# Performance work log

Measured on AMD Instinct MI355X. Metric: run time of the kernel, lower is better.

Reference implementation:

```python
import jax, jax.numpy as jnp
import numpy as np

B = 2          # point-cloud batches
N_PER_B = 8192 # non-empty pillars per batch
C = 128        # channels
H = 4          # heads
K = 4096       # max_tokens (top-k cap)
LN_EPS = 1e-5


def setup_inputs() -> dict:
    key = jax.random.key(0)
    ks = jax.random.split(key, 6)
    N = B * N_PER_B
    feats = jax.random.normal(ks[0], (N, C), dtype=jnp.float32)
    # equal-sized contiguous batch groups (sorted batch ids)
    batch_idx = jnp.repeat(jnp.arange(B, dtype=jnp.int64), N_PER_B)
    in_proj_w = jax.random.normal(ks[1], (3 * C, C), dtype=jnp.float32) * 0.02
    in_proj_b = jax.random.normal(ks[2], (3 * C,), dtype=jnp.float32) * 0.02
    out_proj_w = jax.random.normal(ks[3], (C, C), dtype=jnp.float32) * 0.02
    out_proj_b = jax.random.normal(ks[4], (C,), dtype=jnp.float32) * 0.02
    ln_w = jnp.ones((C,), dtype=jnp.float32)
    ln_b = jnp.zeros((C,), dtype=jnp.float32)
    return {"feats": feats, "batch_idx": batch_idx, "in_proj_w": in_proj_w,
            "in_proj_b": in_proj_b, "out_proj_w": out_proj_w,
            "out_proj_b": out_proj_b, "ln_w": ln_w, "ln_b": ln_b}


def _sparse_pillar_attn(feats, in_proj_w, in_proj_b, out_proj_w, out_proj_b, ln_w, ln_b):
    Dh = C // H
    x = feats.reshape(B, N_PER_B, C)
    # top-K tokens per batch by L2 feature norm (cap at max_tokens)
    norms = jnp.linalg.norm(x, axis=-1)                      # [B, n]
    _, topk = jax.lax.top_k(norms, K)                        # [B, K]
    xa = jnp.take_along_axis(x, topk[..., None], axis=1)     # [B, K, C]
    # MultiheadAttention (batch_first, self-attn)
    qkv = xa @ in_proj_w.T + in_proj_b                       # [B, K, 3C]
    q, k, v = jnp.split(qkv, 3, axis=-1)
    def heads(t):  # [B, K, C] -> [B, H, K, Dh]
        return t.reshape(B, K, H, Dh).transpose(0, 2, 1, 3)
    q, k, v = heads(q), heads(k), heads(v)
    scores = jnp.einsum('bhqd,bhkd->bhqk', q, k) / jnp.sqrt(jnp.float32(Dh))
    attn = jax.nn.softmax(scores, axis=-1)
    o = jnp.einsum('bhqk,bhkd->bhqd', attn, v)               # [B, H, K, Dh]
    o = o.transpose(0, 2, 1, 3).reshape(B, K, C)
    o = o @ out_proj_w.T + out_proj_b
    # residual + LayerNorm (dropout p=0 -> identity)
    h = xa + o
    mu = jnp.mean(h, axis=-1, keepdims=True)
    var = jnp.mean(jnp.square(h - mu), axis=-1, keepdims=True)
    y = (h - mu) / jnp.sqrt(var + LN_EPS) * ln_w + ln_b      # [B, K, C]
    # scatter back; non-selected tokens unchanged
    gidx = (jnp.arange(B)[:, None] * N_PER_B + topk).reshape(-1)
    return feats.at[gidx].set(y.reshape(-1, C))


def reference(feats, batch_idx, in_proj_w, in_proj_b, out_proj_w, out_proj_b, ln_w, ln_b):
    # batch_idx is sorted with equal group sizes, so groups are contiguous
    return _sparse_pillar_attn(feats, in_proj_w, in_proj_b, out_proj_w, out_proj_b, ln_w, ln_b)
```

## Files before the change

### kernel.cpp

```cpp
#include <hip/hip_runtime.h>
#include <hip/hip_bf16.h>
#include <stdint.h>

#define NPB 8192
#define CB 2
#define CC 128
#define HH 4
#define KTOK 4096
#define DH 32
#define NTOK (CB*KTOK)
#define K2C 0.25503402f

typedef __attribute__((ext_vector_type(8))) short sh8;
typedef __attribute__((ext_vector_type(4))) float fx4;
typedef __attribute__((ext_vector_type(16))) float fx16;
typedef __attribute__((ext_vector_type(2))) uint32_t ux2;
typedef __attribute__((ext_vector_type(4))) uint32_t ux4;

__device__ inline uint16_t f2bf(float f){
  uint32_t x = __float_as_uint(f);
  return (uint16_t)((x + 0x7FFFu + ((x>>16)&1u)) >> 16);
}
__device__ inline uint32_t pk2(float a, float b){
  return (uint32_t)f2bf(a) | ((uint32_t)f2bf(b) << 16);
}
__device__ inline float fast_exp2(float x){
#if __has_builtin(__builtin_amdgcn_exp2f)
  return __builtin_amdgcn_exp2f(x);
#else
  return exp2f(x);
#endif
}
__device__ inline uint32_t cvtpk1(float a, float b){
  uint32_t u;
  asm("v_cvt_pk_bf16_f32 %0, %1, %2" : "=v"(u) : "v"(a), "v"(b));
  return u;
}
__device__ inline fx4 mfma32(sh8 a, sh8 b, fx4 c){
  return __builtin_amdgcn_mfma_f32_16x16x32_bf16(a, b, c, 0, 0, 0);
}
__device__ inline fx16 mfma32x32(sh8 a, sh8 b, fx16 c){
  return __builtin_amdgcn_mfma_f32_32x32x16_bf16(a, b, c, 0, 0, 0);
}
__device__ inline void gload_lds(const uint16_t* g, uint16_t* l){
  __builtin_amdgcn_global_load_lds(
      (const __attribute__((address_space(1))) uint32_t*)g,
      (__attribute__((address_space(3))) uint32_t*)l,
      16, 0, 0);
}

__global__ __launch_bounds__(256) void k_cpnw(const float* __restrict__ feats,
                                              float* __restrict__ out,
                                              uint32_t* __restrict__ keys,
                                              const float* __restrict__ wq,
                                              const float* __restrict__ wo,
                                              uint16_t* __restrict__ wqb,
                                              uint16_t* __restrict__ wob){
  int bx = blockIdx.x;
  if (bx < 1024){
    int wv = threadIdx.x >> 6, lane = threadIdx.x & 63;
    int row0 = bx*16 + wv*4;
#pragma unroll
    for (int r = 0; r < 4; ++r){
      int row = row0 + r;
      float2 v = *(const float2*)(feats + row*CC + lane*2);
      *(float2*)(out + row*CC + lane*2) = v;
      float s = v.x*v.x + v.y*v.y;
      for (int m = 1; m < 64; m <<= 1) s += __shfl_xor(s, m);
      if (lane == 0) keys[row] = __float_as_uint(s);
    }
  } else {
    int i = (bx - 1024)*256 + threadIdx.x;
    if (i < 3*CC*CC) wqb[i] = f2bf(wq[i]);
    else { int j = i - 3*CC*CC; wob[j] = f2bf(wo[j]); }
  }
}

__global__ __launch_bounds__(1024) void k_select(const uint32_t* __restrict__ keys,
                                                 int* __restrict__ sel){
  __shared__ uint32_t ka[NPB];
  __shared__ uint32_t hist[16*257];
  __shared__ uint32_t sh_prefix, sh_r;
  __shared__ int wsum[17];
  int tid = threadIdx.x, batch = blockIdx.x;
  int wv16 = tid >> 6;
  for (int i = tid; i < NPB; i += 1024) ka[i] = keys[batch*NPB + i];
  if (tid == 0){ sh_prefix = 0u; sh_r = KTOK; }
  __syncthreads();
  for (int pass = 0; pass < 4; ++pass){
    int shift = 24 - 8*pass;
    for (int i = tid; i < 16*257; i += 1024) hist[i] = 0u;
    __syncthreads();
    uint32_t pref = sh_prefix;
    uint32_t r0   = sh_r;
    uint32_t mask = (pass == 0) ? 0u : (0xFFFFFFFFu << (shift + 8));
    uint32_t* myh = &hist[wv16*257];
    for (int e = 0; e < 8; ++e){
      uint32_t k = ka[tid*8 + e];
      if ((k & mask) == pref) atomicAdd(&myh[(k >> shift) & 255], 1u);
    }
    __syncthreads();
    if (tid < 64){
      int lane = tid;
      uint32_t h0v = 0, h1v = 0, h2v = 0, h3v = 0;
      int b0 = lane*4;
#pragma unroll
      for (int w = 0; w < 16; ++w){
        const uint32_t* hw = &hist[w*257 + b0];
        h0v += hw[0]; h1v += hw[1]; h2v += hw[2]; h3v += hw[3];
      }
      uint32_t s3 = h3v, s2 = h2v + s3, s1 = h1v + s2, s0 = h0v + s1;
      uint32_t incl = s0;
      for (int d = 1; d < 64; d <<= 1){
        uint32_t t = __shfl_down(incl, d);
        if (lane + d < 64) incl += t;
      }
      uint32_t exA = incl - s0;
      uint32_t sfx[4] = {s0, s1, s2, s3};
      uint32_t hh[4]  = {h0v, h1v, h2v, h3v};
#pragma unroll
      for (int k = 0; k < 4; ++k){
        uint32_t inc_b = exA + sfx[k];
        uint32_t Sx    = inc_b - hh[k];
        if (Sx < r0 && inc_b >= r0){
          sh_prefix = pref | ((uint32_t)(b0 + k) << shift);
          sh_r = r0 - Sx;
        }
      }
    }
    __syncthreads();
  }
  uint32_t T = sh_prefix; int need = (int)sh_r;
  int lgt = 0, leq = 0;
  for (int e = 0; e < 8; ++e){
    uint32_t k = ka[tid*8 + e];
    lgt += (k > T); leq += (k == T);
  }
  int lane = tid & 63, wv = tid >> 6;
  int egt, tgt, eeq;
  {
    __syncthreads();
    int incl = lgt;
    for (int d = 1; d < 64; d <<= 1){ int t = __shfl_up(incl, d); if (lane >= d) incl += t; }
    if (lane == 63) wsum[wv] = incl;
    __syncthreads();
    if (tid == 0){ int run = 0; for (int w = 0; w < 16; ++w){ int t = wsum[w]; wsum[w] = run; run += t; } wsum[16] = run; }
    __syncthreads();
    egt = wsum[wv] + incl - lgt; tgt = wsum[16];
  }
  {
    __syncthreads();
    int incl = leq;
    for (int d = 1; d < 64; d <<= 1){ int t = __shfl_up(incl, d); if (lane >= d) incl += t; }
    if (lane == 63) wsum[wv] = incl;
    __syncthreads();
    if (tid == 0){ int run = 0; for (int w = 0; w < 16; ++w){ int t = wsum[w]; wsum[w] = run; run += t; } }
    __syncthreads();
    eeq = wsum[wv] + incl - leq;
  }
  int chi = tgt, gpos = egt, epos = eeq;
  for (int e = 0; e < 8; ++e){
    int i = tid*8 + e;
    uint32_t k = ka[i];
    if (k > T){ sel[batch*KTOK + (gpos++)] = batch*NPB + i; }
    else if (k == T){ if (epos < need) sel[batch*KTOK + chi + epos] = batch*NPB + i; epos++; }
  }
}

__global__ __launch_bounds__(256) void k_qkv(const float* __restrict__ feats,
                                             const int* __restrict__ sel,
                                             const uint16_t* __restrict__ wqb,
                                             const float* __restrict__ bias,
                                             uint16_t* __restrict__ Qg,
                                             uint16_t* __restrict__ Kg,
                                             uint16_t* __restrict__ Vt){
  int wave = threadIdx.x >> 6, lane = threadIdx.x & 63;
  int l15 = lane & 15, g = lane >> 4;
  int rt = blockIdx.x;
  int arow = rt*16 + l15;
  int grow = sel[arow];
  sh8 aF[4];
#pragma unroll
  for (int kk = 0; kk < 4; ++kk){
    const float* src = feats + grow*CC + kk*32 + g*8;
    float4 v0 = *(const float4*)(src);
    float4 v1 = *(const float4*)(src + 4);
    ux4 u;
    u.x = cvtpk1(v0.x, v0.y);
    u.y = cvtpk1(v0.z, v0.w);
    u.z = cvtpk1(v1.x, v1.y);
    u.w = cvtpk1(v1.z, v1.w);
    aF[kk] = *(sh8*)&u;
  }
  int tbase = rt*16;
  int b  = tbase >> 12;
  int q0 = (tbase & 4095) + g*4;
#pragma unroll
  for (int cg = 0; cg < 6; ++cg){
    int bcol = (cg*4 + wave)*16 + l15;
    fx4 acc = {0.f,0.f,0.f,0.f};
#pragma unroll
    for (int kk = 0; kk < 4; ++kk){
      sh8 bF = *(const sh8*)(wqb + bcol*CC + kk*32 + g*8);
      acc = mfma32(aF[kk], bF, acc);
    }
    int j = bcol;
    float bj = bias[j];
    if (j < CC){
      int h = j >> 5, d = j & 31;
      uint16_t* p = Qg + ((b*HH + h)*KTOK + q0)*DH + d;
#pragma unroll
      for (int i = 0; i < 4; ++i) p[i*DH] = f2bf((acc[i] + bj) * K2C);
    } else if (j < 2*CC){
      int jj = j - CC; int h = jj >> 5, d = jj & 31;
      uint16_t* p = Kg + ((b*HH + h)*KTOK + q0)*DH + d;
#pragma unroll
      for (int i = 0; i < 4; ++i) p[i*DH] = f2bf(acc[i] + bj);
    } else {
      int jj = j - 2*CC; int h = jj >> 5, d = jj & 31;
      uint16_t* p = Vt + ((b*HH + h)*DH + d)*KTOK + q0;
      ux2 w; w.x = pk2(acc[0]+bj, acc[1]+bj); w.y = pk2(acc[2]+bj, acc[3]+bj);
      *(ux2*)p = w;
    }
  }
}

__global__ __launch_bounds__(1024) void k_attn(const uint16_t* __restrict__ Qg,
                                               const uint16_t* __restrict__ Kg,
                                               const uint16_t* __restrict__ Vtg,
                                               uint16_t* __restrict__ O){
  __shared__ __align__(16) char lds[68096];
  int tid = threadIdx.x;
  int wv = tid >> 6, lane = tid & 63;
  int l31 = lane & 31, hi = lane >> 5;
  int seg = wv & 3, tq = wv >> 2;
  int bh = blockIdx.y;
  int qt = blockIdx.x;
  const uint16_t* Qp = Qg  + bh*KTOK*DH;
  const uint16_t* Kp = Kg  + bh*KTOK*DH;
  const uint16_t* Vp = Vtg + bh*DH*KTOK;
  int q = qt*128 + tq*32 + l31;
  sh8 qF0 = *(const sh8*)(Qp + q*DH + hi*8);
  sh8 qF1 = *(const sh8*)(Qp + q*DH + 16 + hi*8);

  uint16_t* st = (uint16_t*)lds;
  int r16 = lane >> 2;
  int kr  = (r16 & 3) | ((r16 & 4) << 1) | ((r16 & 8) >> 1);
  int sx  = ((lane & 3) ^ ((r16 >> 1) & 3)) * 8;
  int sseg = wv & 3;
  int skey0 = sseg*1024;

  if (wv < 4){
    const uint16_t* kg = Kp + skey0*DH;
    uint16_t* d = st + sseg*4096;
#pragma unroll
    for (int ks = 0; ks < 2; ++ks){
      gload_lds(kg + (ks*32 + kr)*DH + sx,      d + ks*1024 + 0);
      gload_lds(kg + (ks*32 + 16 + kr)*DH + sx, d + ks*1024 + 512);
    }
  } else if (wv < 8){
    const uint16_t* vg = Vp + skey0;
    uint16_t* d = st + sseg*4096 + 2048;
#pragma unroll
    for (int ks = 0; ks < 2; ++ks){
      gload_lds(vg + r16*KTOK + ks*32 + sx,        d + ks*1024 + 0);
      gload_lds(vg + (16+r16)*KTOK + ks*32 + sx,   d + ks*1024 + 512);
    }
  }
  asm volatile("s_waitcnt vmcnt(0)" ::: "memory");
  __syncthreads();

  fx16 acc  = {0,0,0,0,0,0,0,0,0,0,0,0,0,0,0,0};
  fx16 accl = {0,0,0,0,0,0,0,0,0,0,0,0,0,0,0,0};
  const fx16 z16 = {0,0,0,0,0,0,0,0,0,0,0,0,0,0,0,0};
  const short ONEB = (short)0x3F80;
  sh8 onesB = {ONEB,ONEB,ONEB,ONEB,ONEB,ONEB,ONEB,ONEB};
  int swz = (l31 >> 1) & 3;
  int koff0 = l31*32 + ((hi     ^ swz)*8);
  int koff1 = l31*32 + (((hi+2) ^ swz)*8);

  for (int t = 0; t < 16; ++t){
    int b = t & 1;
    if (t < 15){
      int nk = skey0 + (t+1)*64;
      if (wv < 4){
        const uint16_t* kg = Kp + nk*DH;
        uint16_t* d = st + ((b^1)*4 + sseg)*4096;
#pragma unroll
        for (int ks = 0; ks < 2; ++ks){
          gload_lds(kg + (ks*32 + kr)*DH + sx,      d + ks*1024 + 0);
          gload_lds(kg + (ks*32 + 16 + kr)*DH + sx, d + ks*1024 + 512);
        }
      } else if (wv < 8){
        const uint16_t* vg = Vp + nk;
        uint16_t* d = st + ((b^1)*4 + sseg)*4096 + 2048;
#pragma unroll
        for (int ks = 0; ks < 2; ++ks){
          gload_lds(vg + r16*KTOK + ks*32 + sx,        d + ks*1024 + 0);
          gload_lds(vg + (16+r16)*KTOK + ks*32 + sx,   d + ks*1024 + 512);
        }
      }
    }
    const uint16_t* base = st + (b*4 + seg)*4096;
#pragma unroll
    for (int ks = 0; ks < 2; ++ks){
      const uint16_t* bK = base + ks*1024;
      const uint16_t* bV = base + 2048 + ks*1024;
      sh8 kA0 = *(const sh8*)(bK + koff0);
      sh8 kA1 = *(const sh8*)(bK + koff1);
      fx16 S = mfma32x32(kA0, qF0, z16);
      S = mfma32x32(kA1, qF1, S);
      float e[16];
#pragma unroll
      for (int r = 0; r < 16; ++r) e[r] = fast_exp2(S[r]);
      ux4 w0, w1;
      w0.x = cvtpk1(e[0],  e[1]);  w0.y = cvtpk1(e[2],  e[3]);
      w0.z = cvtpk1(e[4],  e[5]);  w0.w = cvtpk1(e[6],  e[7]);
      w1.x = cvtpk1(e[8],  e[9]);  w1.y = cvtpk1(e[10], e[11]);
      w1.z = cvtpk1(e[12], e[13]); w1.w = cvtpk1(e[14], e[15]);
      sh8 pa0 = *(sh8*)&w0;
      sh8 pa1 = *(sh8*)&w1;
      sh8 vB0 = *(const sh8*)(bV + koff0);
      sh8 vB1 = *(const sh8*)(bV + koff1);
      acc  = mfma32x32(pa0, vB0, acc);
      acc  = mfma32x32(pa1, vB1, acc);
      accl = mfma32x32(pa0, onesB, accl);
      accl = mfma32x32(pa1, onesB, accl);
    }
    asm volatile("s_waitcnt vmcnt(0)" ::: "memory");
    __syncthreads();
  }

  float* cmb = (float*)lds;
  float* lwp = (float*)(lds + 65536);
  float* ltr = (float*)(lds + 65536 + 2048);
#pragma unroll
  for (int i = 0; i < 16; i += 4){
    fx4 p = {acc[i], acc[i+1], acc[i+2], acc[i+3]};
    *(fx4*)&cmb[((tq*4 + seg)*64 + lane)*16 + i] = p;
  }
  if (l31 == 0){
#pragma unroll
    for (int r = 0; r < 16; ++r)
      lwp[wv*32 + (r&3) + 8*(r>>2) + 4*hi] = accl[r];
  }
  __syncthreads();
  if (seg == 0){
#pragma unroll
    for (int s = 1; s < 4; ++s){
#pragma unroll
      for (int i = 0; i < 16; i += 4){
        fx4 p = *(const fx4*)&cmb[((tq*4 + s)*64 + lane)*16 + i];
        acc[i] += p.x; acc[i+1] += p.y; acc[i+2] += p.z; acc[i+3] += p.w;
      }
    }
    float lt = (lwp[(tq*4+0)*32 + l31] + lwp[(tq*4+1)*32 + l31])
             + (lwp[(tq*4+2)*32 + l31] + lwp[(tq*4+3)*32 + l31]);
    if (!hi) ltr[tq*32 + l31] = lt;
    fx4 La = *(const fx4*)&ltr[tq*32 + 4*hi];
    fx4 Lb = *(const fx4*)&ltr[tq*32 + 8 + 4*hi];
    fx4 Lc = *(const fx4*)&ltr[tq*32 + 16 + 4*hi];
    fx4 Ld = *(const fx4*)&ltr[tq*32 + 24 + 4*hi];
    fx4 Ra = {1.f/La.x, 1.f/La.y, 1.f/La.z, 1.f/La.w};
    fx4 Rb = {1.f/Lb.x, 1.f/Lb.y, 1.f/Lb.z, 1.f/Lb.w};
    fx4 Rc = {1.f/Lc.x, 1.f/Lc.y, 1.f/Lc.z, 1.f/Lc.w};
    fx4 Rd = {1.f/Ld.x, 1.f/Ld.y, 1.f/Ld.z, 1.f/Ld.w};
    int bb = bh >> 2, h = bh & 3;
    uint16_t* op = O + (bb*KTOK + qt*128 + tq*32)*CC + h*DH + l31;
#pragma unroll
    for (int r = 0; r < 16; ++r){
      int qd = (r&3) + 8*(r>>2) + 4*hi;
      float rv = (r<4) ? Ra[r&3] : (r<8) ? Rb[r&3] : (r<12) ? Rc[r&3] : Rd[r&3];
      op[qd*CC] = f2bf(acc[r] * rv);
    }
  }
}

__global__ __launch_bounds__(256) void k_outln(const uint16_t* __restrict__ O,
                                               const uint16_t* __restrict__ wob,
                                               const float* __restrict__ bo,
                                               const float* __restrict__ feats,
                                               const int* __restrict__ sel,
                                               const float* __restrict__ lnw,
                                               const float* __restrict__ lnb,
                                               float* __restrict__ out){
  __shared__ float red[16][4][2];
  int wave = threadIdx.x >> 6, lane = threadIdx.x & 63;
  int l15 = lane & 15, g = lane >> 4;
  int rt = blockIdx.x;
  int arow = rt*16 + l15;
  int jA = wave*32 + l15, jB = jA + 16;
  fx4 accA = {0,0,0,0}, accB = {0,0,0,0};
#pragma unroll
  for (int kk = 0; kk < 4; ++kk){
    sh8 aF = *(const sh8*)(O   + arow*CC + kk*32 + g*8);
    sh8 b0 = *(const sh8*)(wob + jA*CC   + kk*32 + g*8);
    sh8 b1 = *(const sh8*)(wob + jB*CC   + kk*32 + g*8);
    accA = mfma32(aF, b0, accA);
    accB = mfma32(aF, b1, accB);
  }
  float bjA = bo[jA], bjB = bo[jB];
  float hA[4], hB[4]; int gl[4];
#pragma unroll
  for (int i = 0; i < 4; ++i){
    int r = rt*16 + g*4 + i;
    int grow = sel[r];
    gl[i] = grow;
    hA[i] = accA[i] + bjA + feats[grow*CC + jA];
    hB[i] = accB[i] + bjB + feats[grow*CC + jB];
  }
#pragma unroll
  for (int i = 0; i < 4; ++i){
    float s  = hA[i] + hB[i];
    float s2 = hA[i]*hA[i] + hB[i]*hB[i];
    for (int mk = 1; mk < 16; mk <<= 1){ s += __shfl_xor(s, mk); s2 += __shfl_xor(s2, mk); }
    if (l15 == 0){ red[g*4+i][wave][0] = s; red[g*4+i][wave][1] = s2; }
  }
  __syncthreads();
  float w0 = lnw[jA], w1 = lnw[jB], b0v = lnb[jA], b1v = lnb[jB];
#pragma unroll
  for (int i = 0; i < 4; ++i){
    int rl = g*4 + i;
    float tot  = red[rl][0][0] + red[rl][1][0] + red[rl][2][0] + red[rl][3][0];
    float tot2 = red[rl][0][1] + red[rl][1][1] + red[rl][2][1] + red[rl][3][1];
    float mu  = tot  * (1.f/128.f);
    float var = tot2 * (1.f/128.f) - mu*mu;
    float rs = rsqrtf(var + 1e-5f);
    out[gl[i]*CC + jA] = (hA[i]-mu)*rs*w0 + b0v;
    out[gl[i]*CC + jB] = (hB[i]-mu)*rs*w1 + b1v;
  }
}

extern "C" void kernel_launch(void* const* d_in, const int* in_sizes, int n_in,
                              void* d_out, int out_size, void* d_ws, size_t ws_size,
                              hipStream_t stream){
  const float* feats = (const float*)d_in[0];
  const float* wqkv  = (const float*)d_in[2];
  const float* bqkv  = (const float*)d_in[3];
  const float* wout  = (const float*)d_in[4];
  const float* bout  = (const float*)d_in[5];
  const float* lnw   = (const float*)d_in[6];
  const float* lnb   = (const float*)d_in[7];
  float* out = (float*)d_out;
  char* ws = (char*)d_ws;

  uint32_t* keys = (uint32_t*)(ws + 0);
  int*      sel  = (int*)     (ws + 65536);
  uint16_t* wqb  = (uint16_t*)(ws + 98304);
  uint16_t* wob  = (uint16_t*)(ws + 196608);
  uint16_t* Qg   = (uint16_t*)(ws + 2326528);
  uint16_t* Kg   = (uint16_t*)(ws + 4423680);
  uint16_t* Vt   = (uint16_t*)(ws + 6520832);
  uint16_t* O    = (uint16_t*)(ws + 8617984);

  hipLaunchKernelGGL(k_cpnw,   dim3(1280),   dim3(256),  0, stream,
                     feats, out, keys, wqkv, wout, wqb, wob);
  hipLaunchKernelGGL(k_select, dim3(2),      dim3(1024), 0, stream, keys, sel);
  hipLaunchKernelGGL(k_qkv,    dim3(512),    dim3(256),  0, stream,
                     feats, sel, wqb, bqkv, Qg, Kg, Vt);
  hipLaunchKernelGGL(k_attn,   dim3(32,8),   dim3(1024), 0, stream, Qg, Kg, Vt, O);
  hipLaunchKernelGGL(k_outln,  dim3(512),    dim3(256),  0, stream, O, wob, bout, feats, sel, lnw, lnb, out);
}
```

Baseline: 71.02 us.

## Copy only unselected rows in output kernel and move weight cast into select

The first kernel no longer copies all of feats into the output. It now only computes the row-norm keys and clears a selection-flag array. The select kernel marks the chosen rows in the flags and uses extra blocks to cast the weights to bf16. The output/LayerNorm kernel gets extra blocks that copy only the unselected rows, which avoids writing the selected half twice and takes the copy off the critical path at the start. The cost is that the flags array must be written and read, and the copy blocks now share the final kernel.

```diff
diff --git a/kernel.cpp b/kernel.cpp
--- a/kernel.cpp
+++ b/kernel.cpp
@@ -49,40 +49,36 @@
       16, 0, 0);
 }
 
-__global__ __launch_bounds__(256) void k_cpnw(const float* __restrict__ feats,
-                                              float* __restrict__ out,
-                                              uint32_t* __restrict__ keys,
-                                              const float* __restrict__ wq,
-                                              const float* __restrict__ wo,
-                                              uint16_t* __restrict__ wqb,
-                                              uint16_t* __restrict__ wob){
-  int bx = blockIdx.x;
-  if (bx < 1024){
-    int wv = threadIdx.x >> 6, lane = threadIdx.x & 63;
-    int row0 = bx*16 + wv*4;
-#pragma unroll
-    for (int r = 0; r < 4; ++r){
-      int row = row0 + r;
-      float2 v = *(const float2*)(feats + row*CC + lane*2);
-      *(float2*)(out + row*CC + lane*2) = v;
-      float s = v.x*v.x + v.y*v.y;
-      for (int m = 1; m < 64; m <<= 1) s += __shfl_xor(s, m);
-      if (lane == 0) keys[row] = __float_as_uint(s);
-    }
-  } else {
-    int i = (bx - 1024)*256 + threadIdx.x;
+__global__ __launch_bounds__(256) void k_norms(const float* __restrict__ feats,
+                                               uint32_t* __restrict__ keys,
+                                               int* __restrict__ flags){
+  if (blockIdx.x < 64) flags[blockIdx.x*256 + threadIdx.x] = 0;
+  int row  = blockIdx.x*4 + (threadIdx.x>>6);
+  int lane = threadIdx.x & 63;
+  float2 v = *(const float2*)(feats + row*CC + lane*2);
+  float s = v.x*v.x + v.y*v.y;
+  for (int m = 1; m < 64; m <<= 1) s += __shfl_xor(s, m);
+  if (lane == 0) keys[row] = __float_as_uint(s);
+}
+
+__global__ __launch_bounds__(1024) void k_select(const uint32_t* __restrict__ keys,
+                                                 int* __restrict__ sel,
+                                                 int* __restrict__ flags,
+                                                 const float* __restrict__ wq,
+                                                 const float* __restrict__ wo,
+                                                 uint16_t* __restrict__ wqb,
+                                                 uint16_t* __restrict__ wob){
+  int tid = threadIdx.x, batch = blockIdx.x;
+  if (batch >= 2){
+    int i = (batch - 2)*1024 + tid;
     if (i < 3*CC*CC) wqb[i] = f2bf(wq[i]);
     else { int j = i - 3*CC*CC; wob[j] = f2bf(wo[j]); }
-  }
-}
-
-__global__ __launch_bounds__(1024) void k_select(const uint32_t* __restrict__ keys,
-                                                 int* __restrict__ sel){
+    return;
+  }
   __shared__ uint32_t ka[NPB];
   __shared__ uint32_t hist[16*257];
   __shared__ uint32_t sh_prefix, sh_r;
   __shared__ int wsum[17];
-  int tid = threadIdx.x, batch = blockIdx.x;
   int wv16 = tid >> 6;
   for (int i = tid; i < NPB; i += 1024) ka[i] = keys[batch*NPB + i];
   if (tid == 0){ sh_prefix = 0u; sh_r = KTOK; }
@@ -162,8 +158,12 @@
   for (int e = 0; e < 8; ++e){
     int i = tid*8 + e;
     uint32_t k = ka[i];
-    if (k > T){ sel[batch*KTOK + (gpos++)] = batch*NPB + i; }
-    else if (k == T){ if (epos < need) sel[batch*KTOK + chi + epos] = batch*NPB + i; epos++; }
+    int grow = batch*NPB + i;
+    if (k > T){ sel[batch*KTOK + (gpos++)] = grow; flags[grow] = 1; }
+    else if (k == T){
+      if (epos < need){ sel[batch*KTOK + chi + epos] = grow; flags[grow] = 1; }
+      epos++;
+    }
   }
 }
 
@@ -381,13 +381,26 @@
                                                const float* __restrict__ bo,
                                                const float* __restrict__ feats,
                                                const int* __restrict__ sel,
+                                               const int* __restrict__ flags,
                                                const float* __restrict__ lnw,
                                                const float* __restrict__ lnb,
                                                float* __restrict__ out){
+  int bx = blockIdx.x;
+  if (bx >= 512){
+    int cb = bx - 512;
+    int row = cb*32 + (threadIdx.x >> 3);
+    int c0  = (threadIdx.x & 7) * 16;
+    if (!flags[row]){
+      const float4* s = (const float4*)(feats + row*CC + c0);
+      float4* d = (float4*)(out + row*CC + c0);
+      d[0] = s[0]; d[1] = s[1]; d[2] = s[2]; d[3] = s[3];
+    }
+    return;
+  }
   __shared__ float red[16][4][2];
   int wave = threadIdx.x >> 6, lane = threadIdx.x & 63;
   int l15 = lane & 15, g = lane >> 4;
-  int rt = blockIdx.x;
+  int rt = bx;
   int arow = rt*16 + l15;
   int jA = wave*32 + l15, jB = jA + 16;
   fx4 accA = {0,0,0,0}, accB = {0,0,0,0};
@@ -448,16 +461,18 @@
   int*      sel  = (int*)     (ws + 65536);
   uint16_t* wqb  = (uint16_t*)(ws + 98304);
   uint16_t* wob  = (uint16_t*)(ws + 196608);
+  int*      flags= (int*)     (ws + 229376);
   uint16_t* Qg   = (uint16_t*)(ws + 2326528);
   uint16_t* Kg   = (uint16_t*)(ws + 4423680);
   uint16_t* Vt   = (uint16_t*)(ws + 6520832);
   uint16_t* O    = (uint16_t*)(ws + 8617984);
 
-  hipLaunchKernelGGL(k_cpnw,   dim3(1280),   dim3(256),  0, stream,
-                     feats, out, keys, wqkv, wout, wqb, wob);
-  hipLaunchKernelGGL(k_select, dim3(2),      dim3(1024), 0, stream, keys, sel);
+  hipLaunchKernelGGL(k_norms,  dim3(4096),   dim3(256),  0, stream, feats, keys, flags);
+  hipLaunchKernelGGL(k_select, dim3(66),     dim3(1024), 0, stream,
+                     keys, sel, flags, wqkv, wout, wqb, wob);
   hipLaunchKernelGGL(k_qkv,    dim3(512),    dim3(256),  0, stream,
                      feats, sel, wqb, bqkv, Qg, Kg, Vt);
   hipLaunchKernelGGL(k_attn,   dim3(32,8),   dim3(1024), 0, stream, Qg, Kg, Vt, O);
-  hipLaunchKernelGGL(k_outln,  dim3(512),    dim3(256),  0, stream, O, wob, bout, feats, sel, lnw, lnb, out);
-}
+  hipLaunchKernelGGL(k_outln,  dim3(1024),   dim3(256),  0, stream,
+                     O, wob, bout, feats, sel, flags, lnw, lnb, out);
+}
```

Result: slower. 72.44 us (+2.0%).
